# Performance work log

Measured on AMD Instinct MI355X. Metric: run time of the kernel, lower is better.

Reference implementation:

```python
import jax, jax.numpy as jnp
import numpy as np

D = 768  # embedding_size

def setup_inputs() -> dict:
    key = jax.random.key(0)
    k1, k2, k3, k4 = jax.random.split(key, 4)
    B, S = 256, 512
    embeddings = jax.random.normal(k1, (B, S, D), dtype=jnp.float32)
    # nn.Linear(768, 1, bias=False).weight -> store as vector [D]
    w_att = jax.random.normal(k2, (D,), dtype=jnp.float32) * (1.0 / np.sqrt(D))
    # nn.Linear(768, 1, bias=True)
    w_pred = jax.random.normal(k3, (D,), dtype=jnp.float32) * (1.0 / np.sqrt(D))
    b_pred = jax.random.normal(k4, (), dtype=jnp.float32) * (1.0 / np.sqrt(D))
    return {"embeddings": embeddings, "w_att": w_att, "w_pred": w_pred, "b_pred": b_pred}

def reference(embeddings, w_att, w_pred, b_pred):
    # Batched attention pooling (the torch code loops over batch; math is identical).
    # Dropout is inference-mode identity.
    scores = jnp.einsum('bsd,d->bs', embeddings, w_att)          # [B, S]
    attn = jax.nn.softmax(scores, axis=-1)                        # [B, S]
    pooled = jnp.einsum('bs,bsd->bd', attn, embeddings)           # [B, D]
    logits = jnp.einsum('bd,d->b', pooled, w_pred) + b_pred       # [B]
    return jax.nn.sigmoid(logits)                                 # [B]
```

## Files before the change

kernel.cpp:

```cpp
#include <hip/hip_runtime.h>
#include <math.h>

#define EMB_D 768
#define SEQ_S 512
#define BLOCK 1024
#define NWAVES (BLOCK / 64)
#define ROWS_PER_WAVE (SEQ_S / NWAVES)
#define RINT 4

__global__ __launch_bounds__(BLOCK, 4) void attn_pool_kernel(
    const float* __restrict__ emb,
    const float* __restrict__ w_att,
    const float* __restrict__ w_pred,
    const float* __restrict__ b_pred,
    float* __restrict__ out)
{
    __shared__ float s_score[SEQ_S];
    __shared__ float s_t[SEQ_S];
    __shared__ float s_red_a[NWAVES];
    __shared__ float s_red_b[NWAVES];

    const int b    = blockIdx.x;
    const int tid  = threadIdx.x;
    const int lane = tid & 63;
    const int wave = tid >> 6;

    const float4* wa4 = (const float4*)w_att;
    const float4* wp4 = (const float4*)w_pred;
    float4 wa[3], wp[3];
#pragma unroll
    for (int c = 0; c < 3; ++c) {
        wa[c] = wa4[lane + 64 * c];
        wp[c] = wp4[lane + 64 * c];
    }

    const float4* e4 = (const float4*)(emb + (size_t)b * SEQ_S * EMB_D);

#pragma unroll 1
    for (int r = 0; r < ROWS_PER_WAVE; r += RINT) {
        const int s0 = wave * ROWS_PER_WAVE + r;

        float4 v[RINT][3];
#pragma unroll
        for (int j = 0; j < RINT; ++j) {
            const float4* row = e4 + (size_t)(s0 + j) * (EMB_D / 4);
#pragma unroll
            for (int c = 0; c < 3; ++c)
                v[j][c] = row[lane + 64 * c];
        }

        float sa[RINT], sp[RINT];
#pragma unroll
        for (int j = 0; j < RINT; ++j) {
            sa[j] = 0.f; sp[j] = 0.f;
#pragma unroll
            for (int c = 0; c < 3; ++c) {
                sa[j] = fmaf(v[j][c].x, wa[c].x, sa[j]);
                sa[j] = fmaf(v[j][c].y, wa[c].y, sa[j]);
                sa[j] = fmaf(v[j][c].z, wa[c].z, sa[j]);
                sa[j] = fmaf(v[j][c].w, wa[c].w, sa[j]);
                sp[j] = fmaf(v[j][c].x, wp[c].x, sp[j]);
                sp[j] = fmaf(v[j][c].y, wp[c].y, sp[j]);
                sp[j] = fmaf(v[j][c].z, wp[c].z, sp[j]);
                sp[j] = fmaf(v[j][c].w, wp[c].w, sp[j]);
            }
        }

#pragma unroll
        for (int off = 32; off > 0; off >>= 1) {
#pragma unroll
            for (int j = 0; j < RINT; ++j) {
                sa[j] += __shfl_down(sa[j], off, 64);
                sp[j] += __shfl_down(sp[j], off, 64);
            }
        }
        if (lane == 0) {
#pragma unroll
            for (int j = 0; j < RINT; ++j) {
                s_score[s0 + j] = sa[j];
                s_t[s0 + j]     = sp[j];
            }
        }
    }
    __syncthreads();

    float score = -INFINITY, tval = 0.f;
    if (tid < SEQ_S) {
        score = s_score[tid];
        tval  = s_t[tid];
    }

    float m = score;
#pragma unroll
    for (int off = 1; off < 64; off <<= 1)
        m = fmaxf(m, __shfl_xor(m, off, 64));
    if (lane == 0) s_red_a[wave] = m;
    __syncthreads();
    if (tid == 0) {
        float mm = s_red_a[0];
#pragma unroll
        for (int w = 1; w < NWAVES; ++w) mm = fmaxf(mm, s_red_a[w]);
        s_red_a[0] = mm;
    }
    __syncthreads();
    m = s_red_a[0];
    __syncthreads();

    float e = (tid < SEQ_S) ? __expf(score - m) : 0.f;
    float se  = e;
    float set = e * tval;
#pragma unroll
    for (int off = 1; off < 64; off <<= 1) {
        se  += __shfl_xor(se, off, 64);
        set += __shfl_xor(set, off, 64);
    }
    if (lane == 0) {
        s_red_a[wave] = se;
        s_red_b[wave] = set;
    }
    __syncthreads();
    if (tid == 0) {
        float Z = 0.f, ET = 0.f;
#pragma unroll
        for (int w = 0; w < NWAVES; ++w) {
            Z  += s_red_a[w];
            ET += s_red_b[w];
        }
        float logit = ET / Z + b_pred[0];
        out[b] = 1.0f / (1.0f + __expf(-logit));
    }
}

extern "C" void kernel_launch(void* const* d_in, const int* in_sizes, int n_in,
                              void* d_out, int out_size, void* d_ws, size_t ws_size,
                              hipStream_t stream) {
    const float* emb    = (const float*)d_in[0];
    const float* w_att  = (const float*)d_in[1];
    const float* w_pred = (const float*)d_in[2];
    const float* b_pred = (const float*)d_in[3];
    float* out = (float*)d_out;

    const int B = in_sizes[0] / (SEQ_S * EMB_D);
    attn_pool_kernel<<<B, BLOCK, 0, stream>>>(emb, w_att, w_pred, b_pred, out);
}
```

Baseline: 523.7 us.

## Split fused kernel into chunked score kernel and per-batch softmax kernel

```diff
diff --git a/kernel.cpp b/kernel.cpp
--- a/kernel.cpp
+++ b/kernel.cpp
@@ -3,27 +3,26 @@
 
 #define EMB_D 768
 #define SEQ_S 512
-#define BLOCK 1024
-#define NWAVES (BLOCK / 64)
-#define ROWS_PER_WAVE (SEQ_S / NWAVES)
+#define NBATCH 256
+#define CHUNKS 16
+#define CHUNK_ROWS (SEQ_S / CHUNKS)
+#define K1_BLOCK 256
+#define K1_WAVES (K1_BLOCK / 64)
+#define ROWS_PER_WAVE (CHUNK_ROWS / K1_WAVES)
 #define RINT 4
 
-__global__ __launch_bounds__(BLOCK, 4) void attn_pool_kernel(
+__global__ __launch_bounds__(K1_BLOCK) void score_kernel(
     const float* __restrict__ emb,
     const float* __restrict__ w_att,
     const float* __restrict__ w_pred,
-    const float* __restrict__ b_pred,
-    float* __restrict__ out)
+    float* __restrict__ scores,
+    float* __restrict__ tvals)
 {
-    __shared__ float s_score[SEQ_S];
-    __shared__ float s_t[SEQ_S];
-    __shared__ float s_red_a[NWAVES];
-    __shared__ float s_red_b[NWAVES];
-
-    const int b    = blockIdx.x;
     const int tid  = threadIdx.x;
     const int lane = tid & 63;
     const int wave = tid >> 6;
+    const int b     = blockIdx.x >> 4;
+    const int chunk = blockIdx.x & 15;
 
     const float4* wa4 = (const float4*)w_att;
     const float4* wp4 = (const float4*)w_pred;
@@ -35,10 +34,11 @@
     }
 
     const float4* e4 = (const float4*)(emb + (size_t)b * SEQ_S * EMB_D);
+    const int s_base = chunk * CHUNK_ROWS + wave * ROWS_PER_WAVE;
 
 #pragma unroll 1
     for (int r = 0; r < ROWS_PER_WAVE; r += RINT) {
-        const int s0 = wave * ROWS_PER_WAVE + r;
+        const int s0 = s_base + r;
 
         float4 v[RINT][3];
 #pragma unroll
@@ -77,18 +77,31 @@
         if (lane == 0) {
 #pragma unroll
             for (int j = 0; j < RINT; ++j) {
-                s_score[s0 + j] = sa[j];
-                s_t[s0 + j]     = sp[j];
+                scores[b * SEQ_S + s0 + j] = sa[j];
+                tvals[b * SEQ_S + s0 + j]  = sp[j];
             }
         }
     }
-    __syncthreads();
+}
 
-    float score = -INFINITY, tval = 0.f;
-    if (tid < SEQ_S) {
-        score = s_score[tid];
-        tval  = s_t[tid];
-    }
+#define K2_BLOCK 512
+#define K2_WAVES (K2_BLOCK / 64)
+__global__ __launch_bounds__(K2_BLOCK) void softmax_kernel(
+    const float* __restrict__ scores,
+    const float* __restrict__ tvals,
+    const float* __restrict__ b_pred,
+    float* __restrict__ out)
+{
+    __shared__ float s_red_a[K2_WAVES];
+    __shared__ float s_red_b[K2_WAVES];
+
+    const int b    = blockIdx.x;
+    const int tid  = threadIdx.x;
+    const int lane = tid & 63;
+    const int wave = tid >> 6;
+
+    float score = scores[b * SEQ_S + tid];
+    float tval  = tvals[b * SEQ_S + tid];
 
     float m = score;
 #pragma unroll
@@ -99,16 +112,15 @@
     if (tid == 0) {
         float mm = s_red_a[0];
 #pragma unroll
-        for (int w = 1; w < NWAVES; ++w) mm = fmaxf(mm, s_red_a[w]);
+        for (int w = 1; w < K2_WAVES; ++w) mm = fmaxf(mm, s_red_a[w]);
         s_red_a[0] = mm;
     }
     __syncthreads();
     m = s_red_a[0];
     __syncthreads();
 
-    float e = (tid < SEQ_S) ? __expf(score - m) : 0.f;
-    float se  = e;
-    float set = e * tval;
+    float e  = __expf(score - m);
+    float se = e, set = e * tval;
 #pragma unroll
     for (int off = 1; off < 64; off <<= 1) {
         se  += __shfl_xor(se, off, 64);
@@ -122,7 +134,7 @@
     if (tid == 0) {
         float Z = 0.f, ET = 0.f;
 #pragma unroll
-        for (int w = 0; w < NWAVES; ++w) {
+        for (int w = 0; w < K2_WAVES; ++w) {
             Z  += s_red_a[w];
             ET += s_red_b[w];
         }
@@ -141,5 +153,9 @@
     float* out = (float*)d_out;
 
     const int B = in_sizes[0] / (SEQ_S * EMB_D);
-    attn_pool_kernel<<<B, BLOCK, 0, stream>>>(emb, w_att, w_pred, b_pred, out);
+    float* scores = (float*)d_ws;
+    float* tvals  = scores + (size_t)B * SEQ_S;
+
+    score_kernel<<<B * CHUNKS, K1_BLOCK, 0, stream>>>(emb, w_att, w_pred, scores, tvals);
+    softmax_kernel<<<B, K2_BLOCK, 0, stream>>>(scores, tvals, b_pred, out);
 }
```

Measured after the change: 520.7 us. About the same (-0.6%).
